# Performance work log

Hardware: AMD Instinct MI355X
Metric: run time of the kernel (lower is better)

Reference implementation:

```python
import jax, jax.numpy as jnp
import numpy as np

N_NODES = 50000
N_EDGES = 1600000
IN_DIM = 128
HID = 128
SHARED = 64
N_GRAPHS = 2048


def setup_inputs() -> dict:
    key = jax.random.key(0)
    ks = jax.random.split(key, 16)
    x = jax.random.normal(ks[0], (N_NODES, IN_DIM), dtype=jnp.float32)
    edge_index = jax.random.randint(ks[1], (2, N_EDGES), 0, N_NODES, dtype=jnp.int64)
    batch = jnp.sort(jax.random.randint(ks[2], (N_NODES,), 0, N_GRAPHS, dtype=jnp.int64))

    def lin(k, fan_in, fan_out):
        bound = 1.0 / np.sqrt(fan_in)
        kw, kb = jax.random.split(k)
        W = jax.random.uniform(kw, (fan_in, fan_out), minval=-bound, maxval=bound, dtype=jnp.float32)
        b = jax.random.uniform(kb, (fan_out,), minval=-bound, maxval=bound, dtype=jnp.float32)
        return W, b

    W1a, b1a = lin(ks[3], IN_DIM, HID)
    W1b, b1b = lin(ks[4], HID, HID)
    W2a, b2a = lin(ks[5], HID, HID)
    W2b, b2b = lin(ks[6], HID, HID)
    Ws, bs = lin(ks[7], HID, SHARED)
    WlS, blS = lin(ks[8], SHARED, 1)
    WlP, blP = lin(ks[9], SHARED, 1)
    WnR, bnR = lin(ks[10], SHARED, 1)
    return dict(x=x, edge_index=edge_index, batch=batch,
                W1a=W1a, b1a=b1a, W1b=W1b, b1b=b1b,
                W2a=W2a, b2a=b2a, W2b=W2b, b2b=b2b,
                Ws=Ws, bs=bs, WlS=WlS, blS=blS, WlP=WlP, blP=blP, WnR=WnR, bnR=bnR)


def gin_conv(x, src, dst, Wa, ba, Wb, bb):
    # GINConv (eps=0): h_i = MLP(x_i + sum_{j->i} x_j)
    agg = jax.ops.segment_sum(x[src], dst, num_segments=N_NODES)
    h = x + agg
    h = jax.nn.relu(h @ Wa + ba)
    return h @ Wb + bb


def reference(x, edge_index, batch, W1a, b1a, W1b, b1b, W2a, b2a, W2b, b2b,
              Ws, bs, WlS, blS, WlP, blP, WnR, bnR):
    src, dst = edge_index[0], edge_index[1]
    h = jax.nn.relu(gin_conv(x, src, dst, W1a, b1a, W1b, b1b))
    h = jax.nn.relu(gin_conv(h, src, dst, W2a, b2a, W2b, b2b))
    # global mean pool over graph ids
    sums = jax.ops.segment_sum(h, batch, num_segments=N_GRAPHS)
    counts = jax.ops.segment_sum(jnp.ones((h.shape[0],), h.dtype), batch, num_segments=N_GRAPHS)
    pooled = sums / jnp.maximum(counts, 1.0)[:, None]
    g = jax.nn.relu(pooled @ Ws + bs)
    out_logS = (g @ WlS + blS)[:, 0]
    out_logP = (g @ WlP + blP)[:, 0]
    out_NR = (g @ WnR + bnR)[:, 0]
    return (out_logS, out_logP, out_NR)
```

## Files before the change

kernel.cpp:

```cpp
#include <hip/hip_runtime.h>
#include <hip/hip_bf16.h>


#define IN_DIM 128
#define NFINE 128
#define BIN_EPB 4096
#define SRCCH 16
#define NSLOT 6400
#define SPT 13

typedef float  f32x4  __attribute__((ext_vector_type(4)));
typedef short  bf16x4 __attribute__((ext_vector_type(4)));
typedef short  bf16x8 __attribute__((ext_vector_type(8)));

__device__ __forceinline__ unsigned short bf16_rne(float v) {
    unsigned u = __float_as_uint(v);
    unsigned t = u + 0x7fffu + ((u >> 16) & 1u);
    return (unsigned short)(t >> 16);
}


__global__ __launch_bounds__(256) void f32_to_bf16_kernel(
    const float4* __restrict__ in, uint4* __restrict__ out, int n8)
{
    int i = blockIdx.x * 256 + threadIdx.x;
    if (i >= n8) return;
    float4 a = in[i * 2];
    float4 b = in[i * 2 + 1];
    float v[8] = {a.x, a.y, a.z, a.w, b.x, b.y, b.z, b.w};
    unsigned r[4];
#pragma unroll
    for (int j = 0; j < 4; ++j)
        r[j] = (unsigned)bf16_rne(v[j * 2]) | ((unsigned)bf16_rne(v[j * 2 + 1]) << 16);
    out[i] = make_uint4(r[0], r[1], r[2], r[3]);
}


__global__ __launch_bounds__(256) void conv_weights_kernel(
    const float* __restrict__ W0, const float* __restrict__ W1,
    const float* __restrict__ W2, const float* __restrict__ W3,
    unsigned short* __restrict__ Wh, unsigned short* __restrict__ Wl)
{
    int m   = blockIdx.x >> 6;
    int idx = (blockIdx.x & 63) * 256 + threadIdx.x;
    const float* W = (m == 0) ? W0 : (m == 1) ? W1 : (m == 2) ? W2 : W3;
    int k = idx >> 7, n = idx & 127;
    float v = W[idx];
    unsigned short hh = bf16_rne(v);
    float hf = __uint_as_float(((unsigned)hh) << 16);
    unsigned short ll = bf16_rne(v - hf);
    Wh[m * 16384 + n * 128 + k] = hh;
    Wl[m * 16384 + n * 128 + k] = ll;
}


__global__ __launch_bounds__(256) void bin_kernel(
    const int* __restrict__ src, const int* __restrict__ dst,
    int2* __restrict__ buckets, int* __restrict__ bcur,
    int n_edges, int n_nodes, int cap)
{
    __shared__ int cnt[NFINE];
    __shared__ int base[NFINE];
    for (int i = threadIdx.x; i < NFINE; i += 256) cnt[i] = 0;
    __syncthreads();

    const int e0 = blockIdx.x * BIN_EPB + threadIdx.x * 16;
    int ne = n_edges - e0;
    if (ne < 0) ne = 0;
    if (ne > 16) ne = 16;

    int d[16], s[16], off[16];
    if (ne == 16) {
#pragma unroll
        for (int q = 0; q < 4; ++q) {
            int4 dv = *(const int4*)(dst + e0 + q * 4);
            int4 sv = *(const int4*)(src + e0 + q * 4);
            d[q * 4 + 0] = dv.x; d[q * 4 + 1] = dv.y;
            d[q * 4 + 2] = dv.z; d[q * 4 + 3] = dv.w;
            s[q * 4 + 0] = sv.x; s[q * 4 + 1] = sv.y;
            s[q * 4 + 2] = sv.z; s[q * 4 + 3] = sv.w;
        }
    } else {
#pragma unroll
        for (int j = 0; j < 16; ++j) {
            d[j] = (j < ne) ? dst[e0 + j] : 0;
            s[j] = (j < ne) ? src[e0 + j] : 0;
        }
    }
#pragma unroll
    for (int j = 0; j < 16; ++j)
        if (j < ne) {
            int b = (int)(((long long)d[j] * NFINE) / n_nodes);
            off[j] = atomicAdd(&cnt[b], 1);
        }
    __syncthreads();
    for (int i = threadIdx.x; i < NFINE; i += 256)
        base[i] = atomicAdd(&bcur[i], cnt[i]);
    __syncthreads();
#pragma unroll
    for (int j = 0; j < 16; ++j)
        if (j < ne) {
            int b = (int)(((long long)d[j] * NFINE) / n_nodes);
            buckets[(size_t)b * cap + base[b] + off[j]] = make_int2(d[j], s[j]);
        }
}

__global__ __launch_bounds__(512) void csr_fused_kernel(
    const int2* __restrict__ buckets, const int* __restrict__ bcnt,
    int* __restrict__ row_start, int* __restrict__ csr_src,
    int cap, int n_nodes, int n_edges)
{
    __shared__ int bc[NFINE];
    __shared__ int h[NSLOT];
    __shared__ int tsum[512];
    __shared__ int bbase_s;

    const int b = blockIdx.x;
    const int t = threadIdx.x;
    const int lo_n = (int)(((long long)b * n_nodes + NFINE - 1) / NFINE);
    const int hi_n = (int)(((long long)(b + 1) * n_nodes + NFINE - 1) / NFINE);
    const int sl = hi_n - lo_n;

    if (t < NFINE) bc[t] = bcnt[t];
    for (int i = t; i < NSLOT; i += 512) h[i] = 0;
    __syncthreads();
    if (t == 0) {
        int s = 0;
        for (int i = 0; i < b; ++i) s += bc[i];
        bbase_s = s;
    }
    const int nb = bc[b];
    const int2* bp = buckets + (size_t)b * cap;
    __syncthreads();

    for (int i = t; i < nb; i += 512) {
        int2 e = bp[i];
        int key = (e.x - lo_n) * SRCCH + (int)(((long long)e.y * SRCCH) / n_nodes);
        atomicAdd(&h[key], 1);
    }
    __syncthreads();

    int base = 0;
#pragma unroll
    for (int j = 0; j < SPT; ++j) {
        int slot = t * SPT + j;
        if (slot < NSLOT) {
            int v = h[slot];
            h[slot] = base;
            base += v;
        }
    }
    tsum[t] = base;
    __syncthreads();
    for (int off = 1; off < 512; off <<= 1) {
        int tmp = (t >= off) ? tsum[t - off] : 0;
        __syncthreads();
        tsum[t] += tmp;
        __syncthreads();
    }
    int texcl = tsum[t] - base + bbase_s;
#pragma unroll
    for (int j = 0; j < SPT; ++j) {
        int slot = t * SPT + j;
        if (slot < NSLOT) h[slot] += texcl;
    }
    __syncthreads();
    for (int i = t; i < sl; i += 512) row_start[lo_n + i] = h[i * SRCCH];
    if (b == NFINE - 1 && t == 0) row_start[n_nodes] = n_edges;
    __syncthreads();

    for (int i = t; i < nb; i += 512) {
        int2 e = bp[i];
        int key = (e.x - lo_n) * SRCCH + (int)(((long long)e.y * SRCCH) / n_nodes);
        csr_src[atomicAdd(&h[key], 1)] = e.y;
    }
}

#define HSTRIDE 132

__device__ __forceinline__ void add_row8(float acc[8], uint4 r) {
    union { unsigned u; float f; } c;
    c.u = r.x << 16;         acc[0] += c.f;
    c.u = r.x & 0xffff0000u; acc[1] += c.f;
    c.u = r.y << 16;         acc[2] += c.f;
    c.u = r.y & 0xffff0000u; acc[3] += c.f;
    c.u = r.z << 16;         acc[4] += c.f;
    c.u = r.z & 0xffff0000u; acc[5] += c.f;
    c.u = r.w << 16;         acc[6] += c.f;
    c.u = r.w & 0xffff0000u; acc[7] += c.f;
}

template <int LAYER>
__global__ __launch_bounds__(512) void fused_gin_layer_kernel(
    const float* __restrict__ xf,
    const uint4* __restrict__ selfh,
    const uint4* __restrict__ selfl,
    const uint4* __restrict__ nbr,
    const int* __restrict__ row_start, const int* __restrict__ csr_src,
    const unsigned short* __restrict__ Wa_h, const unsigned short* __restrict__ Wa_l,
    const float* __restrict__ ba,
    const unsigned short* __restrict__ Wb_h, const unsigned short* __restrict__ Wb_l,
    const float* __restrict__ bb,
    float* __restrict__ C, unsigned short* __restrict__ Ch,
    unsigned short* __restrict__ Cl, int M)
{
    __shared__ __align__(16) unsigned short Hh[64][HSTRIDE];
    __shared__ __align__(16) unsigned short Hl[64][HSTRIDE];

    const int t    = threadIdx.x;
    const int brow = blockIdx.x * 64;

    {
        const int lane = t & 15;
        const int gr   = t >> 4;
#pragma unroll
        for (int it = 0; it < 2; ++it) {
            const int rl   = it * 32 + gr;
            const int node = brow + rl;
            float acc[8] = {0.f, 0.f, 0.f, 0.f, 0.f, 0.f, 0.f, 0.f};
            if (node < M) {
                if constexpr (LAYER == 1) {
                    const f32x4* xfr = (const f32x4*)(xf + (size_t)node * IN_DIM + lane * 8);
                    f32x4 a0 = xfr[0];
                    f32x4 a1 = xfr[1];
                    acc[0] = a0.x; acc[1] = a0.y; acc[2] = a0.z; acc[3] = a0.w;
                    acc[4] = a1.x; acc[5] = a1.y; acc[6] = a1.z; acc[7] = a1.w;
                } else {
                    add_row8(acc, selfh[(size_t)node * 16 + lane]);
                    add_row8(acc, selfl[(size_t)node * 16 + lane]);
                }
                const int lo = row_start[node];
                const int hi = row_start[node + 1];
                int e = lo;
                for (; e + 3 < hi; e += 4) {
                    int s0 = csr_src[e];
                    int s1 = csr_src[e + 1];
                    int s2 = csr_src[e + 2];
                    int s3 = csr_src[e + 3];
                    uint4 r0 = nbr[(size_t)s0 * 16 + lane];
                    uint4 r1 = nbr[(size_t)s1 * 16 + lane];
                    uint4 r2 = nbr[(size_t)s2 * 16 + lane];
                    uint4 r3 = nbr[(size_t)s3 * 16 + lane];
                    add_row8(acc, r0);
                    add_row8(acc, r1);
                    add_row8(acc, r2);
                    add_row8(acc, r3);
                }
                for (; e < hi; ++e)
                    add_row8(acc, nbr[(size_t)csr_src[e] * 16 + lane]);
            }
            unsigned short hh[8], ll[8];
#pragma unroll
            for (int j = 0; j < 8; ++j) {
                unsigned short h = bf16_rne(acc[j]);
                hh[j] = h;
                ll[j] = bf16_rne(acc[j] - __uint_as_float(((unsigned)h) << 16));
            }
            *(bf16x4*)&Hh[rl][lane * 8]     = *(const bf16x4*)&hh[0];
            *(bf16x4*)&Hh[rl][lane * 8 + 4] = *(const bf16x4*)&hh[4];
            *(bf16x4*)&Hl[rl][lane * 8]     = *(const bf16x4*)&ll[0];
            *(bf16x4*)&Hl[rl][lane * 8 + 4] = *(const bf16x4*)&ll[4];
        }
    }
    __syncthreads();

    const int wave = t >> 6;
    const int lane = t & 63;
    const int l15  = lane & 15;
    const int quad = lane >> 4;
    const int rh   = (wave & 1) * 32;
    const int cq   = (wave >> 1) * 32;

    f32x4 acc[2][2];
#pragma unroll
    for (int ti = 0; ti < 2; ++ti)
#pragma unroll
        for (int ct = 0; ct < 2; ++ct) acc[ti][ct] = {0.f, 0.f, 0.f, 0.f};

#pragma unroll
    for (int k0 = 0; k0 < IN_DIM; k0 += 32) {
        const int hk = k0 + quad * 8;
        bf16x8 ah[2], al[2];
#pragma unroll
        for (int ti = 0; ti < 2; ++ti) {
            const int hr = rh + ti * 16 + l15;
            bf16x4 h0 = *(const bf16x4*)&Hh[hr][hk];
            bf16x4 h1 = *(const bf16x4*)&Hh[hr][hk + 4];
            bf16x4 l0 = *(const bf16x4*)&Hl[hr][hk];
            bf16x4 l1 = *(const bf16x4*)&Hl[hr][hk + 4];
            ah[ti] = __builtin_shufflevector(h0, h1, 0, 1, 2, 3, 4, 5, 6, 7);
            al[ti] = __builtin_shufflevector(l0, l1, 0, 1, 2, 3, 4, 5, 6, 7);
        }
#pragma unroll
        for (int ct = 0; ct < 2; ++ct) {
            const size_t woff = (size_t)(cq + ct * 16 + l15) * IN_DIM + k0 + quad * 8;
            bf16x8 wh = *(const bf16x8*)(Wa_h + woff);
            bf16x8 wl = *(const bf16x8*)(Wa_l + woff);
            acc[0][ct] = __builtin_amdgcn_mfma_f32_16x16x32_bf16(ah[0], wh, acc[0][ct], 0, 0, 0);
            acc[1][ct] = __builtin_amdgcn_mfma_f32_16x16x32_bf16(ah[1], wh, acc[1][ct], 0, 0, 0);
            acc[0][ct] = __builtin_amdgcn_mfma_f32_16x16x32_bf16(al[0], wh, acc[0][ct], 0, 0, 0);
            acc[1][ct] = __builtin_amdgcn_mfma_f32_16x16x32_bf16(al[1], wh, acc[1][ct], 0, 0, 0);
            acc[0][ct] = __builtin_amdgcn_mfma_f32_16x16x32_bf16(ah[0], wl, acc[0][ct], 0, 0, 0);
            acc[1][ct] = __builtin_amdgcn_mfma_f32_16x16x32_bf16(ah[1], wl, acc[1][ct], 0, 0, 0);
        }
    }
    __syncthreads();

#pragma unroll
    for (int ti = 0; ti < 2; ++ti) {
#pragma unroll
        for (int ct = 0; ct < 2; ++ct) {
            int col = cq + ct * 16 + l15;
            float b = ba[col];
#pragma unroll
            for (int r = 0; r < 4; ++r) {
                int rl = rh + ti * 16 + quad * 4 + r;
                float v = fmaxf(acc[ti][ct][r] + b, 0.f);
                unsigned short hh = bf16_rne(v);
                Hh[rl][col] = hh;
                Hl[rl][col] = bf16_rne(v - __uint_as_float(((unsigned)hh) << 16));
            }
            acc[ti][ct] = {0.f, 0.f, 0.f, 0.f};
        }
    }
    __syncthreads();

#pragma unroll
    for (int k0 = 0; k0 < IN_DIM; k0 += 32) {
        const int hk = k0 + quad * 8;
        bf16x8 ah[2], al[2];
#pragma unroll
        for (int ti = 0; ti < 2; ++ti) {
            const int hr = rh + ti * 16 + l15;
            bf16x4 h0 = *(const bf16x4*)&Hh[hr][hk];
            bf16x4 h1 = *(const bf16x4*)&Hh[hr][hk + 4];
            bf16x4 l0 = *(const bf16x4*)&Hl[hr][hk];
            bf16x4 l1 = *(const bf16x4*)&Hl[hr][hk + 4];
            ah[ti] = __builtin_shufflevector(h0, h1, 0, 1, 2, 3, 4, 5, 6, 7);
            al[ti] = __builtin_shufflevector(l0, l1, 0, 1, 2, 3, 4, 5, 6, 7);
        }
#pragma unroll
        for (int ct = 0; ct < 2; ++ct) {
            const size_t woff = (size_t)(cq + ct * 16 + l15) * IN_DIM + k0 + quad * 8;
            bf16x8 wh = *(const bf16x8*)(Wb_h + woff);
            bf16x8 wl = *(const bf16x8*)(Wb_l + woff);
            acc[0][ct] = __builtin_amdgcn_mfma_f32_16x16x32_bf16(ah[0], wh, acc[0][ct], 0, 0, 0);
            acc[1][ct] = __builtin_amdgcn_mfma_f32_16x16x32_bf16(ah[1], wh, acc[1][ct], 0, 0, 0);
            acc[0][ct] = __builtin_amdgcn_mfma_f32_16x16x32_bf16(al[0], wh, acc[0][ct], 0, 0, 0);
            acc[1][ct] = __builtin_amdgcn_mfma_f32_16x16x32_bf16(al[1], wh, acc[1][ct], 0, 0, 0);
            acc[0][ct] = __builtin_amdgcn_mfma_f32_16x16x32_bf16(ah[0], wl, acc[0][ct], 0, 0, 0);
            acc[1][ct] = __builtin_amdgcn_mfma_f32_16x16x32_bf16(ah[1], wl, acc[1][ct], 0, 0, 0);
        }
    }

#pragma unroll
    for (int ti = 0; ti < 2; ++ti) {
        const int rbase = brow + rh + ti * 16 + quad * 4;
#pragma unroll
        for (int ct = 0; ct < 2; ++ct) {
            int col = cq + ct * 16 + l15;
            float b = bb[col];
#pragma unroll
            for (int r = 0; r < 4; ++r) {
                int row = rbase + r;
                if (row < M) {
                    float o = fmaxf(acc[ti][ct][r] + b, 0.f);
                    if constexpr (LAYER == 1) {
                        unsigned short hh = bf16_rne(o);
                        Ch[(size_t)row * IN_DIM + col] = hh;
                        Cl[(size_t)row * IN_DIM + col] =
                            bf16_rne(o - __uint_as_float(((unsigned)hh) << 16));
                    } else {
                        C[(size_t)row * IN_DIM + col] = o;
                    }
                }
            }
        }
    }
}


__device__ __forceinline__ int lower_bound_i(const int* __restrict__ a, int n, int v) {
    int lo = 0, hi = n;
    while (lo < hi) {
        int mid = (lo + hi) >> 1;
        if (a[mid] < v) lo = mid + 1; else hi = mid;
    }
    return lo;
}

__global__ __launch_bounds__(128) void pool_kernel(
    const float* __restrict__ h, const int* __restrict__ batch,
    float* __restrict__ pooled, int n_nodes, int n_graphs)
{
    int g = blockIdx.x;
    int lo = lower_bound_i(batch, n_nodes, g);
    int hi = lower_bound_i(batch, n_nodes, g + 1);
    int j = threadIdx.x;
    float acc = 0.f;
    for (int i = lo; i < hi; ++i)
        acc += h[(size_t)i * IN_DIM + j];
    float cnt = (float)(hi - lo);
    pooled[(size_t)g * IN_DIM + j] = acc / fmaxf(cnt, 1.0f);
}

__global__ __launch_bounds__(64) void head_kernel(
    const float* __restrict__ pooled,
    const float* __restrict__ Ws,  const float* __restrict__ bs,
    const float* __restrict__ WlS, const float* __restrict__ blS,
    const float* __restrict__ WlP, const float* __restrict__ blP,
    const float* __restrict__ WnR, const float* __restrict__ bnR,
    float* __restrict__ out, int n_graphs)
{
    int g = blockIdx.x;
    int j = threadIdx.x;
    const float* p = pooled + (size_t)g * IN_DIM;
    float acc = bs[j];
#pragma unroll 8
    for (int k = 0; k < IN_DIM; ++k)
        acc = fmaf(p[k], Ws[k * 64 + j], acc);
    float gj = fmaxf(acc, 0.f);
    float s1 = gj * WlS[j];
    float s2 = gj * WlP[j];
    float s3 = gj * WnR[j];
#pragma unroll
    for (int off = 32; off > 0; off >>= 1) {
        s1 += __shfl_down(s1, off);
        s2 += __shfl_down(s2, off);
        s3 += __shfl_down(s3, off);
    }
    if (j == 0) {
        out[g]                = s1 + blS[0];
        out[n_graphs + g]     = s2 + blP[0];
        out[2 * n_graphs + g] = s3 + bnR[0];
    }
}


extern "C" void kernel_launch(void* const* d_in, const int* in_sizes, int n_in,
                              void* d_out, int out_size, void* d_ws, size_t ws_size,
                              hipStream_t stream)
{
    const float* x   = (const float*)d_in[0];
    const int*   ei  = (const int*)d_in[1];
    const int*   bat = (const int*)d_in[2];
    const float* W1a = (const float*)d_in[3];
    const float* b1a = (const float*)d_in[4];
    const float* W1b = (const float*)d_in[5];
    const float* b1b = (const float*)d_in[6];
    const float* W2a = (const float*)d_in[7];
    const float* b2a = (const float*)d_in[8];
    const float* W2b = (const float*)d_in[9];
    const float* b2b = (const float*)d_in[10];
    const float* Ws  = (const float*)d_in[11];
    const float* bs  = (const float*)d_in[12];
    const float* WlS = (const float*)d_in[13];
    const float* blS = (const float*)d_in[14];
    const float* WlP = (const float*)d_in[15];
    const float* blP = (const float*)d_in[16];
    const float* WnR = (const float*)d_in[17];
    const float* bnR = (const float*)d_in[18];

    const int n_nodes  = in_sizes[0] / IN_DIM;
    const int n_edges  = in_sizes[1] / 2;
    const int n_graphs = out_size / 3;
    const int* src = ei;
    const int* dst = ei + n_edges;

    const size_t node_elems   = (size_t)n_nodes * IN_DIM;
    const size_t pooled_elems = (size_t)n_graphs * IN_DIM;

    unsigned short* xb = (unsigned short*)d_ws;
    unsigned short* Ch = xb + node_elems;
    unsigned short* Cl = Ch + node_elems;
    float* P3     = (float*)(Cl + node_elems);
    float* pooled = P3 + node_elems;
    int* row_start = (int*)(pooled + pooled_elems);
    int* bcur      = row_start + (n_nodes + 1);
    int* csr_src   = bcur + NFINE;
    unsigned short* wt_h = (unsigned short*)(csr_src + n_edges);
    unsigned short* wt_l = wt_h + 4 * 16384;

    const int cap = n_edges / NFINE + 2048;
    int2* buckets = (int2*)P3;

    const int layerblocks = (n_nodes + 63) / 64;
    const int binblocks = (n_edges + BIN_EPB - 1) / BIN_EPB;
    const int n8 = (int)(node_elems / 8);
    const int cvtblocks = (n8 + 255) / 256;

    conv_weights_kernel<<<256, 256, 0, stream>>>(W1a, W1b, W2a, W2b, wt_h, wt_l);
    hipMemsetAsync(bcur, 0, NFINE * sizeof(int), stream);
    bin_kernel<<<binblocks, 256, 0, stream>>>(src, dst, buckets, bcur,
                                              n_edges, n_nodes, cap);
    csr_fused_kernel<<<NFINE, 512, 0, stream>>>(buckets, bcur, row_start,
                                                csr_src, cap, n_nodes, n_edges);
    f32_to_bf16_kernel<<<cvtblocks, 256, 0, stream>>>((const float4*)x, (uint4*)xb, n8);

    fused_gin_layer_kernel<1><<<layerblocks, 512, 0, stream>>>(
        x, nullptr, nullptr, (const uint4*)xb, row_start, csr_src,
        wt_h, wt_l, b1a, wt_h + 16384, wt_l + 16384, b1b,
        nullptr, Ch, Cl, n_nodes);

    fused_gin_layer_kernel<2><<<layerblocks, 512, 0, stream>>>(
        nullptr, (const uint4*)Ch, (const uint4*)Cl, (const uint4*)Ch,
        row_start, csr_src,
        wt_h + 2 * 16384, wt_l + 2 * 16384, b2a,
        wt_h + 3 * 16384, wt_l + 3 * 16384, b2b,
        P3, nullptr, nullptr, n_nodes);

    pool_kernel<<<n_graphs, 128, 0, stream>>>(P3, bat, pooled, n_nodes, n_graphs);
    head_kernel<<<n_graphs, 64, 0, stream>>>(pooled, Ws, bs, WlS, blS, WlP, blP,
                                             WnR, bnR, (float*)d_out, n_graphs);
}
```

Baseline: 344.0 us.

## Gather neighbors in source-chunk phases with block barriers for cache locality

The CSR build now exports per-node, per-source-chunk offsets (16 chunks per node). The GIN layer's aggregation handles both of a thread's nodes together in 8 phases, each covering two source chunks, with a block-wide barrier after every phase. This keeps the threads of a block gathering from the same source-node range at once, so neighbor rows are more likely to be reused in L2/LLC. The cost is extra barriers, load imbalance inside each phase, predicated tail handling, and an extra rcs array that is written and read.

```diff
diff --git a/kernel.cpp b/kernel.cpp
--- a/kernel.cpp
+++ b/kernel.cpp
@@ -107,7 +107,8 @@
 
 __global__ __launch_bounds__(512) void csr_fused_kernel(
     const int2* __restrict__ buckets, const int* __restrict__ bcnt,
-    int* __restrict__ row_start, int* __restrict__ csr_src,
+    int* __restrict__ row_start, int* __restrict__ rcs,
+    int* __restrict__ csr_src,
     int cap, int n_nodes, int n_edges)
 {
     __shared__ int bc[NFINE];
@@ -166,6 +167,7 @@
     }
     __syncthreads();
     for (int i = t; i < sl; i += 512) row_start[lo_n + i] = h[i * SRCCH];
+    for (int i = t; i < sl * SRCCH; i += 512) rcs[lo_n * SRCCH + i] = h[i];
     if (b == NFINE - 1 && t == 0) row_start[n_nodes] = n_edges;
     __syncthreads();
 
@@ -190,13 +192,37 @@
     c.u = r.w & 0xffff0000u; acc[7] += c.f;
 }
 
+__device__ __forceinline__ void gather_range(
+    const int* __restrict__ csr_src, const uint4* __restrict__ nbr,
+    int lane, int s, int e, float acc[8])
+{
+    for (int i = s; i < e; i += 4) {
+        int i1 = (i + 1 < e) ? i + 1 : e - 1;
+        int i2 = (i + 2 < e) ? i + 2 : e - 1;
+        int i3 = (i + 3 < e) ? i + 3 : e - 1;
+        int s0 = csr_src[i];
+        int s1 = csr_src[i1];
+        int s2 = csr_src[i2];
+        int s3 = csr_src[i3];
+        uint4 r0 = nbr[(size_t)s0 * 16 + lane];
+        uint4 r1 = nbr[(size_t)s1 * 16 + lane];
+        uint4 r2 = nbr[(size_t)s2 * 16 + lane];
+        uint4 r3 = nbr[(size_t)s3 * 16 + lane];
+        add_row8(acc, r0);
+        if (i + 1 < e) add_row8(acc, r1);
+        if (i + 2 < e) add_row8(acc, r2);
+        if (i + 3 < e) add_row8(acc, r3);
+    }
+}
+
 template <int LAYER>
 __global__ __launch_bounds__(512) void fused_gin_layer_kernel(
     const float* __restrict__ xf,
     const uint4* __restrict__ selfh,
     const uint4* __restrict__ selfl,
     const uint4* __restrict__ nbr,
-    const int* __restrict__ row_start, const int* __restrict__ csr_src,
+    const int* __restrict__ row_start, const int* __restrict__ rcs,
+    const int* __restrict__ csr_src,
     const unsigned short* __restrict__ Wa_h, const unsigned short* __restrict__ Wa_l,
     const float* __restrict__ ba,
     const unsigned short* __restrict__ Wb_h, const unsigned short* __restrict__ Wb_l,
@@ -211,56 +237,76 @@
     const int brow = blockIdx.x * 64;
 
     {
-        const int lane = t & 15;
-        const int gr   = t >> 4;
-#pragma unroll
-        for (int it = 0; it < 2; ++it) {
-            const int rl   = it * 32 + gr;
-            const int node = brow + rl;
-            float acc[8] = {0.f, 0.f, 0.f, 0.f, 0.f, 0.f, 0.f, 0.f};
-            if (node < M) {
-                if constexpr (LAYER == 1) {
-                    const f32x4* xfr = (const f32x4*)(xf + (size_t)node * IN_DIM + lane * 8);
-                    f32x4 a0 = xfr[0];
-                    f32x4 a1 = xfr[1];
-                    acc[0] = a0.x; acc[1] = a0.y; acc[2] = a0.z; acc[3] = a0.w;
-                    acc[4] = a1.x; acc[5] = a1.y; acc[6] = a1.z; acc[7] = a1.w;
-                } else {
-                    add_row8(acc, selfh[(size_t)node * 16 + lane]);
-                    add_row8(acc, selfl[(size_t)node * 16 + lane]);
-                }
-                const int lo = row_start[node];
-                const int hi = row_start[node + 1];
-                int e = lo;
-                for (; e + 3 < hi; e += 4) {
-                    int s0 = csr_src[e];
-                    int s1 = csr_src[e + 1];
-                    int s2 = csr_src[e + 2];
-                    int s3 = csr_src[e + 3];
-                    uint4 r0 = nbr[(size_t)s0 * 16 + lane];
-                    uint4 r1 = nbr[(size_t)s1 * 16 + lane];
-                    uint4 r2 = nbr[(size_t)s2 * 16 + lane];
-                    uint4 r3 = nbr[(size_t)s3 * 16 + lane];
-                    add_row8(acc, r0);
-                    add_row8(acc, r1);
-                    add_row8(acc, r2);
-                    add_row8(acc, r3);
-                }
-                for (; e < hi; ++e)
-                    add_row8(acc, nbr[(size_t)csr_src[e] * 16 + lane]);
+        const int lane  = t & 15;
+        const int gr    = t >> 4;
+        const int node0 = brow + gr;
+        const int node1 = brow + 32 + gr;
+        const bool val0 = node0 < M;
+        const bool val1 = node1 < M;
+
+        float acc0[8] = {0.f, 0.f, 0.f, 0.f, 0.f, 0.f, 0.f, 0.f};
+        float acc1[8] = {0.f, 0.f, 0.f, 0.f, 0.f, 0.f, 0.f, 0.f};
+        if (val0) {
+            if constexpr (LAYER == 1) {
+                const f32x4* p = (const f32x4*)(xf + (size_t)node0 * IN_DIM + lane * 8);
+                f32x4 a0 = p[0], a1 = p[1];
+                acc0[0] = a0.x; acc0[1] = a0.y; acc0[2] = a0.z; acc0[3] = a0.w;
+                acc0[4] = a1.x; acc0[5] = a1.y; acc0[6] = a1.z; acc0[7] = a1.w;
+            } else {
+                add_row8(acc0, selfh[(size_t)node0 * 16 + lane]);
+                add_row8(acc0, selfl[(size_t)node0 * 16 + lane]);
             }
-            unsigned short hh[8], ll[8];
-#pragma unroll
-            for (int j = 0; j < 8; ++j) {
-                unsigned short h = bf16_rne(acc[j]);
-                hh[j] = h;
-                ll[j] = bf16_rne(acc[j] - __uint_as_float(((unsigned)h) << 16));
+        }
+        if (val1) {
+            if constexpr (LAYER == 1) {
+                const f32x4* p = (const f32x4*)(xf + (size_t)node1 * IN_DIM + lane * 8);
+                f32x4 a0 = p[0], a1 = p[1];
+                acc1[0] = a0.x; acc1[1] = a0.y; acc1[2] = a0.z; acc1[3] = a0.w;
+                acc1[4] = a1.x; acc1[5] = a1.y; acc1[6] = a1.z; acc1[7] = a1.w;
+            } else {
+                add_row8(acc1, selfh[(size_t)node1 * 16 + lane]);
+                add_row8(acc1, selfl[(size_t)node1 * 16 + lane]);
             }
-            *(bf16x4*)&Hh[rl][lane * 8]     = *(const bf16x4*)&hh[0];
-            *(bf16x4*)&Hh[rl][lane * 8 + 4] = *(const bf16x4*)&hh[4];
-            *(bf16x4*)&Hl[rl][lane * 8]     = *(const bf16x4*)&ll[0];
-            *(bf16x4*)&Hl[rl][lane * 8 + 4] = *(const bf16x4*)&ll[4];
-        }
+        }
+
+        const int end0 = val0 ? row_start[node0 + 1] : 0;
+        const int end1 = val1 ? row_start[node1 + 1] : 0;
+        int cur0 = val0 ? rcs[node0 * SRCCH] : 0;
+        int cur1 = val1 ? rcs[node1 * SRCCH] : 0;
+
+#pragma unroll 1
+        for (int cp = 0; cp < 8; ++cp) {
+            int e0 = 0, e1 = 0;
+            if (val0) e0 = (cp < 7) ? rcs[node0 * SRCCH + cp * 2 + 2] : end0;
+            if (val1) e1 = (cp < 7) ? rcs[node1 * SRCCH + cp * 2 + 2] : end1;
+            gather_range(csr_src, nbr, lane, cur0, e0, acc0);
+            gather_range(csr_src, nbr, lane, cur1, e1, acc1);
+            cur0 = e0;
+            cur1 = e1;
+            __syncthreads();
+        }
+
+        unsigned short hh[8], ll[8];
+#pragma unroll
+        for (int j = 0; j < 8; ++j) {
+            unsigned short h = bf16_rne(acc0[j]);
+            hh[j] = h;
+            ll[j] = bf16_rne(acc0[j] - __uint_as_float(((unsigned)h) << 16));
+        }
+        *(bf16x4*)&Hh[gr][lane * 8]     = *(const bf16x4*)&hh[0];
+        *(bf16x4*)&Hh[gr][lane * 8 + 4] = *(const bf16x4*)&hh[4];
+        *(bf16x4*)&Hl[gr][lane * 8]     = *(const bf16x4*)&ll[0];
+        *(bf16x4*)&Hl[gr][lane * 8 + 4] = *(const bf16x4*)&ll[4];
+#pragma unroll
+        for (int j = 0; j < 8; ++j) {
+            unsigned short h = bf16_rne(acc1[j]);
+            hh[j] = h;
+            ll[j] = bf16_rne(acc1[j] - __uint_as_float(((unsigned)h) << 16));
+        }
+        *(bf16x4*)&Hh[gr + 32][lane * 8]     = *(const bf16x4*)&hh[0];
+        *(bf16x4*)&Hh[gr + 32][lane * 8 + 4] = *(const bf16x4*)&hh[4];
+        *(bf16x4*)&Hl[gr + 32][lane * 8]     = *(const bf16x4*)&ll[0];
+        *(bf16x4*)&Hl[gr + 32][lane * 8 + 4] = *(const bf16x4*)&ll[4];
     }
     __syncthreads();
 
@@ -480,6 +526,7 @@
     int* csr_src   = bcur + NFINE;
     unsigned short* wt_h = (unsigned short*)(csr_src + n_edges);
     unsigned short* wt_l = wt_h + 4 * 16384;
+    int* rcs       = (int*)(wt_l + 4 * 16384);
 
     const int cap = n_edges / NFINE + 2048;
     int2* buckets = (int2*)P3;
@@ -493,18 +540,18 @@
     hipMemsetAsync(bcur, 0, NFINE * sizeof(int), stream);
     bin_kernel<<<binblocks, 256, 0, stream>>>(src, dst, buckets, bcur,
                                               n_edges, n_nodes, cap);
-    csr_fused_kernel<<<NFINE, 512, 0, stream>>>(buckets, bcur, row_start,
+    csr_fused_kernel<<<NFINE, 512, 0, stream>>>(buckets, bcur, row_start, rcs,
                                                 csr_src, cap, n_nodes, n_edges);
     f32_to_bf16_kernel<<<cvtblocks, 256, 0, stream>>>((const float4*)x, (uint4*)xb, n8);
 
     fused_gin_layer_kernel<1><<<layerblocks, 512, 0, stream>>>(
-        x, nullptr, nullptr, (const uint4*)xb, row_start, csr_src,
+        x, nullptr, nullptr, (const uint4*)xb, row_start, rcs, csr_src,
         wt_h, wt_l, b1a, wt_h + 16384, wt_l + 16384, b1b,
         nullptr, Ch, Cl, n_nodes);
 
     fused_gin_layer_kernel<2><<<layerblocks, 512, 0, stream>>>(
         nullptr, (const uint4*)Ch, (const uint4*)Cl, (const uint4*)Ch,
-        row_start, csr_src,
+        row_start, rcs, csr_src,
         wt_h + 2 * 16384, wt_l + 2 * 16384, b2a,
         wt_h + 3 * 16384, wt_l + 3 * 16384, b2b,
         P3, nullptr, nullptr, n_nodes);
```

Result: slower. 371.3 us (+7.9%).
